# Kernel tuning notes

Measured on AMD Instinct MI355X. Metric: run time of the kernel, lower is better.

Reference implementation:

```python
import jax, jax.numpy as jnp
import numpy as np

D_MODEL = 1024
N_HEADS = 16
D_H = D_MODEL // N_HEADS
MAX_LEN = 2048
BATCH = 2
SEQ = 2048
EPS = 1e-8
W_SCALE = 0.02


def _rms_norm(x, w):
    # RMSNorm: x * rsqrt(mean(x^2) + eps) * w
    ms = jnp.mean(jnp.square(x), axis=-1, keepdims=True)
    return w * (x * jax.lax.rsqrt(ms + EPS))


def setup_inputs() -> dict:
    key = jax.random.key(0)
    ks = jax.random.split(key, 12)
    d = D_MODEL
    inp = {
        "x": jax.random.normal(ks[0], (BATCH, SEQ, d), dtype=jnp.float32),
        "t_bias": jnp.zeros((1,), dtype=jnp.float32),  # unused by the module
        "p_bias": jax.random.normal(ks[1], (MAX_LEN, N_HEADS), dtype=jnp.float32),
        # AMS layer params (Linear stored as [in, out])
        "wq": jax.random.normal(ks[2], (d, d), dtype=jnp.float32) * W_SCALE,
        "bq": jnp.zeros((d,), dtype=jnp.float32),
        "wk": jax.random.normal(ks[3], (d, d), dtype=jnp.float32) * W_SCALE,
        "bk": jnp.zeros((d,), dtype=jnp.float32),
        "wv": jax.random.normal(ks[4], (d, d), dtype=jnp.float32) * W_SCALE,
        "bv": jnp.zeros((d,), dtype=jnp.float32),
        "wu": jax.random.normal(ks[5], (d, d), dtype=jnp.float32) * W_SCALE,
        "bu": jnp.zeros((d,), dtype=jnp.float32),
        "g_ams": jnp.ones((d,), dtype=jnp.float32),   # shared RMSNorm weight in AMSLayer
        # MFFN layer params
        "w0": jax.random.normal(ks[6], (d, d), dtype=jnp.float32) * W_SCALE,
        "b0": jnp.zeros((d,), dtype=jnp.float32),
        "w1": jax.random.normal(ks[7], (d, 2 * d), dtype=jnp.float32) * W_SCALE,
        "b1": jnp.zeros((2 * d,), dtype=jnp.float32),
        "w2": jax.random.normal(ks[8], (d, d), dtype=jnp.float32) * W_SCALE,
        "b2": jnp.zeros((d,), dtype=jnp.float32),
        "g_mffn": jnp.ones((d,), dtype=jnp.float32),
    }
    return inp


def reference(x, t_bias, p_bias, wq, bq, wk, bk, wv, bv, wu, bu, g_ams,
              w0, b0, w1, b1, w2, b2, g_mffn):
    B, S, d = x.shape
    H, dh = N_HEADS, D_H

    # ---- AMS layer ----
    x_norm = _rms_norm(x, g_ams)

    def proj(w, b):
        # [B,S,d] -> [B,H,S,dh]
        return (x_norm @ w + b).reshape(B, S, H, dh).transpose(0, 2, 1, 3)

    q = proj(wq, bq)
    k = proj(wk, bk)
    v = proj(wv, bv)

    scale = 1.0 / np.sqrt(dh).astype(np.float32)
    score = jnp.einsum('bhsd,bhtd->bhst', q, k) * scale
    # additive positional bias: p_bias[:S].T -> [H,S], broadcast over query dim
    score = score + p_bias[:S, :].T[None, :, None, :]

    attn = jax.nn.silu(score)                        # SiLU instead of softmax
    out = jnp.einsum('bhst,bhtd->bhsd', attn, v)
    out = out.transpose(0, 2, 1, 3).reshape(B, S, d)

    u = jax.nn.silu(x_norm @ wu + bu)
    ams_out = _rms_norm(out, g_ams) * u

    # ---- MFFN layer ----
    o = (ams_out @ w0 + b0) + x
    o_norm = _rms_norm(o, g_mffn)
    x12 = o_norm @ w1 + b1
    x1, x2 = jnp.split(x12, 2, axis=-1)
    swiglu = jax.nn.silu(x1) * x2
    return (swiglu @ w2 + b2) + o
```

## Files before the change

### kernel.cpp

```cpp
#include <hip/hip_runtime.h>
#include <stdint.h>
#include <math.h>


#define D    1024
#define NH   16
#define DH   64
#define B_   2
#define S_   2048
#define ROWS 4096
#define LQ   4096
#define EPSR 1e-8f

typedef unsigned short u16;
typedef __attribute__((ext_vector_type(8))) short short8;
typedef __attribute__((ext_vector_type(4))) float f32x4;
typedef __attribute__((ext_vector_type(16))) float f32x16;
typedef __attribute__((ext_vector_type(4))) int int4v;

__device__ __forceinline__ float bf2f(u16 u) {
    union { uint32_t i; float f; } c; c.i = ((uint32_t)u) << 16; return c.f;
}
__device__ __forceinline__ u16 f2bf(float f) {
    union { float f; uint32_t i; } c; c.f = f;
    uint32_t x = c.i;
    x += 0x7fffu + ((x >> 16) & 1u);
    return (u16)(x >> 16);
}
#define LOG2E 1.44269504f
__device__ __forceinline__ float silu_fast(float v) {
    return v * __builtin_amdgcn_rcpf(1.0f + __builtin_amdgcn_exp2f(v * -LOG2E));
}

__global__ __launch_bounds__(256) void transpose_all_kernel(
    const float* __restrict__ wq, const float* __restrict__ wk,
    const float* __restrict__ wv, const float* __restrict__ wu,
    const float* __restrict__ w0, const float* __restrict__ w2,
    const float* __restrict__ w1,
    u16* __restrict__ wT4, u16* __restrict__ w0T,
    u16* __restrict__ w2T, u16* __restrict__ w1T)
{
    const unsigned MI = 1u << 20;
    const int z = blockIdx.z;
    const float* W; u16* WT; int N; int noff = 0;
    switch (z) {
        case 0: W = wq; WT = wT4;          N = 1024; break;
        case 1: W = wk; WT = wT4 + 1 * MI; N = 1024; break;
        case 2: W = wv; WT = wT4 + 2 * MI; N = 1024; break;
        case 3: W = wu; WT = wT4 + 3 * MI; N = 1024; break;
        case 4: W = w0; WT = w0T;          N = 1024; break;
        case 5: W = w2; WT = w2T;          N = 1024; break;
        case 6: W = w1; WT = w1T;          N = 2048; noff = 0;    break;
        default:W = w1; WT = w1T;          N = 2048; noff = 1024; break;
    }
    __shared__ float T[64][65];
    const int tid = threadIdx.x;
    const int n0 = (blockIdx.x << 6) + noff;
    const int k0 = blockIdx.y << 6;
    const int rr = tid >> 4;
    const int cc = (tid & 15) << 2;
#pragma unroll
    for (int l = 0; l < 4; ++l) {
        const int r = rr + (l << 4);
        float4 v = *(const float4*)&W[(size_t)(k0 + r) * N + n0 + cc];
        T[cc + 0][r] = v.x; T[cc + 1][r] = v.y;
        T[cc + 2][r] = v.z; T[cc + 3][r] = v.w;
    }
    __syncthreads();
    const int n  = tid >> 2;
    const int ks = (tid & 3) << 4;
#pragma unroll
    for (int m = 0; m < 4; ++m) {
        const int k = ks + (m << 2);
        float4 v = *(const float4*)&T[n][k];
        ushort4 o;
        o.x = f2bf(v.x); o.y = f2bf(v.y); o.z = f2bf(v.z); o.w = f2bf(v.w);
        *(ushort4*)&WT[(size_t)(n0 + n) * 1024 + k0 + k] = o;
    }
}

__global__ __launch_bounds__(256) void pbt_kernel(
    const float* __restrict__ pb, float* __restrict__ pbT)
{
    const int tid = threadIdx.x;
    const int r = (blockIdx.x << 7) + (tid >> 1);
    const int c0 = (tid & 1) << 3;
    float4 v0 = *(const float4*)&pb[(size_t)r * NH + c0];
    float4 v1 = *(const float4*)&pb[(size_t)r * NH + c0 + 4];
    pbT[(size_t)(c0 + 0) * S_ + r] = v0.x;
    pbT[(size_t)(c0 + 1) * S_ + r] = v0.y;
    pbT[(size_t)(c0 + 2) * S_ + r] = v0.z;
    pbT[(size_t)(c0 + 3) * S_ + r] = v0.w;
    pbT[(size_t)(c0 + 4) * S_ + r] = v1.x;
    pbT[(size_t)(c0 + 5) * S_ + r] = v1.y;
    pbT[(size_t)(c0 + 6) * S_ + r] = v1.z;
    pbT[(size_t)(c0 + 7) * S_ + r] = v1.w;
}

__global__ __launch_bounds__(256) void rmsnorm_kernel(
    const float* __restrict__ inf, const u16* __restrict__ inb, int ldi,
    const float* __restrict__ g,
    const u16* __restrict__ mul, int ldm,
    u16* __restrict__ out, int ldo)
{
    const int row = blockIdx.x;
    const int tid = threadIdx.x;
    const int c = tid << 2;
    float x0, x1, x2, x3;
    if (inb) {
        ushort4 xi = *(const ushort4*)&inb[(size_t)row * ldi + c];
        x0 = bf2f(xi.x); x1 = bf2f(xi.y); x2 = bf2f(xi.z); x3 = bf2f(xi.w);
    } else {
        float4 xi = *(const float4*)&inf[(size_t)row * ldi + c];
        x0 = xi.x; x1 = xi.y; x2 = xi.z; x3 = xi.w;
    }
    float ss = x0*x0 + x1*x1 + x2*x2 + x3*x3;
#pragma unroll
    for (int off = 32; off > 0; off >>= 1) ss += __shfl_down(ss, off, 64);
    __shared__ float red[4];
    if ((tid & 63) == 0) red[tid >> 6] = ss;
    __syncthreads();
    float r = rsqrtf((red[0] + red[1] + red[2] + red[3]) * (1.0f / D) + EPSR);
    float4 gv = *(const float4*)&g[c];
    float v0 = x0 * r * gv.x, v1 = x1 * r * gv.y, v2 = x2 * r * gv.z, v3 = x3 * r * gv.w;
    if (mul) {
        ushort4 mi = *(const ushort4*)&mul[(size_t)row * ldm + c];
        v0 *= bf2f(mi.x); v1 *= bf2f(mi.y); v2 *= bf2f(mi.z); v3 *= bf2f(mi.w);
    }
    ushort4 o;
    o.x = f2bf(v0); o.y = f2bf(v1); o.z = f2bf(v2); o.w = f2bf(v3);
    *(ushort4*)&out[(size_t)row * ldo + c] = o;
}

__global__ __launch_bounds__(256) void gemm128(
    const u16* __restrict__ A, const u16* __restrict__ WT,
    const float* __restrict__ bs0, const float* __restrict__ bs1,
    const float* __restrict__ bs2, const float* __restrict__ bs3,
    u16* __restrict__ outb, int ldo, int actmask,
    u16* __restrict__ VT, int vtsel)
{
    __shared__ u16 As[128 * 32];
    __shared__ u16 Bs[128 * 32];
    const int tid  = threadIdx.x;
    const int wave = tid >> 6;
    const int lane = tid & 63;
    const int lm   = lane & 15;
    const int quad = lane >> 4;
    const int row0 = blockIdx.y << 7;
    const int col0 = blockIdx.x << 7;
    const int wr = (wave >> 1) << 6;
    const int wc = (wave & 1) << 6;

    const int srow = wave * 32 + (lane >> 2);
    const int skp  = (lane & 3) << 3;
    const u16* Ag = A  + (size_t)(row0 + srow) * 1024 + skp;
    const u16* Bg = WT + (size_t)(col0 + srow) * 1024 + skp;
    u16* Asd0 = &As[(wave * 32) * 32];
    u16* Asd1 = &As[(wave * 32 + 16) * 32];
    u16* Bsd0 = &Bs[(wave * 32) * 32];
    u16* Bsd1 = &Bs[(wave * 32 + 16) * 32];

    f32x4 acc[4][4] = {};

    for (int k0 = 0; k0 < 1024; k0 += 32) {
        __syncthreads();
        __builtin_amdgcn_global_load_lds(
            (const __attribute__((address_space(1))) void*)(Ag + k0),
            (__attribute__((address_space(3))) void*)Asd0, 16, 0, 0);
        __builtin_amdgcn_global_load_lds(
            (const __attribute__((address_space(1))) void*)(Ag + 16 * 1024 + k0),
            (__attribute__((address_space(3))) void*)Asd1, 16, 0, 0);
        __builtin_amdgcn_global_load_lds(
            (const __attribute__((address_space(1))) void*)(Bg + k0),
            (__attribute__((address_space(3))) void*)Bsd0, 16, 0, 0);
        __builtin_amdgcn_global_load_lds(
            (const __attribute__((address_space(1))) void*)(Bg + 16 * 1024 + k0),
            (__attribute__((address_space(3))) void*)Bsd1, 16, 0, 0);
        __syncthreads();
        short8 af[4], bf[4];
#pragma unroll
        for (int i = 0; i < 4; ++i)
            af[i] = *(const short8*)&As[(wr + i * 16 + lm) * 32 + quad * 8];
#pragma unroll
        for (int j = 0; j < 4; ++j)
            bf[j] = *(const short8*)&Bs[(wc + j * 16 + lm) * 32 + quad * 8];
#pragma unroll
        for (int i = 0; i < 4; ++i)
#pragma unroll
            for (int j = 0; j < 4; ++j)
                acc[i][j] = __builtin_amdgcn_mfma_f32_16x16x32_bf16(af[i], bf[j], acc[i][j], 0, 0, 0);
    }
    const int sel = col0 >> 10;
    const float* bias = (sel == 0) ? bs0 : (sel == 1) ? bs1 : (sel == 2) ? bs2 : bs3;
    const int act = (actmask >> sel) & 1;
    if (VT && sel == vtsel) {
        const int b = row0 >> 11;
#pragma unroll
        for (int j = 0; j < 4; ++j) {
            const int c2 = (col0 + wc + j * 16 + lm) & 1023;
            const int h  = c2 >> 6;
            const int dh = c2 & 63;
            const float bj = bias[c2];
            u16* vrow = VT + ((size_t)(b * NH + h) * 64 + dh) * (size_t)S_;
#pragma unroll
            for (int i = 0; i < 4; ++i) {
                const int tb = (row0 & 2047) + wr + i * 16 + quad * 4;
                ushort4 o;
                o.x = f2bf(acc[i][j][0] + bj);
                o.y = f2bf(acc[i][j][1] + bj);
                o.z = f2bf(acc[i][j][2] + bj);
                o.w = f2bf(acc[i][j][3] + bj);
                *(ushort4*)&vrow[tb] = o;
            }
        }
    } else {
#pragma unroll
        for (int j = 0; j < 4; ++j) {
            const int colg = col0 + wc + j * 16 + lm;
            const float bj = bias[colg & 1023];
#pragma unroll
            for (int i = 0; i < 4; ++i) {
#pragma unroll
                for (int r = 0; r < 4; ++r) {
                    const int rowg = row0 + wr + i * 16 + quad * 4 + r;
                    float v = acc[i][j][r] + bj;
                    if (act) v = silu_fast(v);
                    outb[(size_t)rowg * ldo + colg] = f2bf(v);
                }
            }
        }
    }
}

__global__ __launch_bounds__(256) void gemm64(
    const u16* __restrict__ A, int lda, const u16* __restrict__ WT,
    const float* __restrict__ bias,
    const float* __restrict__ res,
    float* __restrict__ outf, int ldo)
{
    __shared__ u16 As[128 * 32];
    __shared__ u16 Bs[64 * 32];
    const int tid  = threadIdx.x;
    const int wave = tid >> 6;
    const int lane = tid & 63;
    const int lm   = lane & 15;
    const int quad = lane >> 4;
    const int row0 = blockIdx.y << 7;
    const int col0 = blockIdx.x << 6;
    const int wr = (wave >> 1) << 6;
    const int wc = (wave & 1) << 5;

    const int srA = wave * 32 + (lane >> 2);
    const int srB = wave * 16 + (lane >> 2);
    const int skp = (lane & 3) << 3;
    const u16* Ag = A  + (size_t)(row0 + srA) * lda + skp;
    const u16* Bg = WT + (size_t)(col0 + srB) * 1024 + skp;
    u16* Asd0 = &As[(wave * 32) * 32];
    u16* Asd1 = &As[(wave * 32 + 16) * 32];
    u16* Bsd  = &Bs[(wave * 16) * 32];

    f32x4 acc[4][2] = {};

    for (int k0 = 0; k0 < 1024; k0 += 32) {
        __syncthreads();
        __builtin_amdgcn_global_load_lds(
            (const __attribute__((address_space(1))) void*)(Ag + k0),
            (__attribute__((address_space(3))) void*)Asd0, 16, 0, 0);
        __builtin_amdgcn_global_load_lds(
            (const __attribute__((address_space(1))) void*)(Ag + (size_t)16 * lda + k0),
            (__attribute__((address_space(3))) void*)Asd1, 16, 0, 0);
        __builtin_amdgcn_global_load_lds(
            (const __attribute__((address_space(1))) void*)(Bg + k0),
            (__attribute__((address_space(3))) void*)Bsd, 16, 0, 0);
        __syncthreads();
        short8 af[4], bf[2];
#pragma unroll
        for (int i = 0; i < 4; ++i)
            af[i] = *(const short8*)&As[(wr + i * 16 + lm) * 32 + quad * 8];
#pragma unroll
        for (int j = 0; j < 2; ++j)
            bf[j] = *(const short8*)&Bs[(wc + j * 16 + lm) * 32 + quad * 8];
#pragma unroll
        for (int i = 0; i < 4; ++i)
#pragma unroll
            for (int j = 0; j < 2; ++j)
                acc[i][j] = __builtin_amdgcn_mfma_f32_16x16x32_bf16(af[i], bf[j], acc[i][j], 0, 0, 0);
    }
#pragma unroll
    for (int j = 0; j < 2; ++j) {
        const int colg = col0 + wc + j * 16 + lm;
        const float bj = bias[colg];
#pragma unroll
        for (int i = 0; i < 4; ++i) {
#pragma unroll
            for (int r = 0; r < 4; ++r) {
                const int rowg = row0 + wr + i * 16 + quad * 4 + r;
                const size_t idx = (size_t)rowg * ldo + colg;
                float v = acc[i][j][r] + bj;
                if (res) v += res[idx];
                outf[idx] = v;
            }
        }
    }
}

__global__ __launch_bounds__(256, 4) void attn_mfma(
    const u16* __restrict__ qkvu, const u16* __restrict__ VT,
    const float* __restrict__ pbT, u16* __restrict__ out)
{
    __shared__ u16 Ks[2][64 * 64];
    __shared__ u16 Vs[2][64 * 64];
    __shared__ float pbl[S_];
    const int tid  = threadIdx.x;
    const int wave = tid >> 6;
    const int lane = tid & 63;
    const int l31  = lane & 31;
    const int hi   = lane >> 5;
    const int l7   = lane & 7;
    const int flat = blockIdx.x + (blockIdx.y << 4) + (blockIdx.z << 8);
    const int work = ((flat & 7) << 6) + (flat >> 3);
    const int s0 = (work & 15) << 7;
    const int h  = (work >> 4) & 15;
    const int b  = work >> 8;
    const size_t base = (size_t)b * S_ * LQ + (size_t)h * DH;
    const u16* q  = qkvu + base;
    const u16* kg = qkvu + base + 1024;
    const u16* vt = VT + (size_t)(b * NH + h) * 64 * S_;
    const float* pbh = pbT + (size_t)h * S_;

    for (int i = tid * 4; i < S_; i += 1024)
        *(float4*)&pbl[i] = *(const float4*)&pbh[i];

    const int qrow = s0 + wave * 32 + l31;
    short8 qf[4];
#pragma unroll
    for (int i = 0; i < 4; ++i)
        qf[i] = *(const short8*)&q[(size_t)qrow * LQ + i * 16 + hi * 8];

    const int lr  = lane >> 3;
    const int gch = l7 ^ lr;
    const u16* kg0 = kg + (size_t)(16 * wave + lr) * LQ + gch * 8;
    const u16* vg0 = vt + (size_t)(16 * wave + lr) * S_ + gch * 8;

#define GLDS(gp, lp) __builtin_amdgcn_global_load_lds( \
        (const __attribute__((address_space(1))) void*)(gp), \
        (__attribute__((address_space(3))) void*)(lp), 16, 0, 0)

    GLDS(kg0,                     &Ks[0][(16 * wave) * 64]);
    GLDS(kg0 + (size_t)8 * LQ,    &Ks[0][(16 * wave + 8) * 64]);
    GLDS(vg0,                     &Vs[0][(16 * wave) * 64]);
    GLDS(vg0 + (size_t)8 * S_,    &Vs[0][(16 * wave + 8) * 64]);

    f32x16 accO[2] = {};
    __syncthreads();

    for (int t0 = 0; t0 < S_; t0 += 64) {
        const int ib = (t0 >> 6) & 1;
        const int nb = ib ^ 1;
        if (t0 + 64 < S_) {
            const size_t tn = (size_t)(t0 + 64);
            GLDS(kg0 + tn * LQ,             &Ks[nb][(16 * wave) * 64]);
            GLDS(kg0 + (tn + 8) * LQ,       &Ks[nb][(16 * wave + 8) * 64]);
            GLDS(vg0 + tn,                  &Vs[nb][(16 * wave) * 64]);
            GLDS(vg0 + tn + (size_t)8 * S_, &Vs[nb][(16 * wave + 8) * 64]);
        }
#pragma unroll
        for (int half = 0; half < 2; ++half) {
            const int ts = half << 5;
            f32x16 st = {};
            __builtin_amdgcn_s_setprio(1);
#pragma unroll
            for (int i = 0; i < 4; ++i) {
                short8 kf = *(const short8*)&Ks[ib][(ts + l31) * 64 + (((2 * i + hi) ^ l7) << 3)];
                st = __builtin_amdgcn_mfma_f32_32x32x16_bf16(kf, qf[i], st, 0, 0, 0);
            }
            __builtin_amdgcn_s_setprio(0);
            int pk[8];
#pragma unroll
            for (int g = 0; g < 4; ++g) {
                float4 pbv = *(const float4*)&pbl[t0 + ts + 8 * g + 4 * hi];
                float p0 = silu_fast(fmaf(st[4 * g + 0], 0.125f, pbv.x));
                float p1 = silu_fast(fmaf(st[4 * g + 1], 0.125f, pbv.y));
                float p2 = silu_fast(fmaf(st[4 * g + 2], 0.125f, pbv.z));
                float p3 = silu_fast(fmaf(st[4 * g + 3], 0.125f, pbv.w));
                asm("v_cvt_pk_bf16_f32 %0, %1, %2" : "=v"(pk[2 * g])     : "v"(p0), "v"(p1));
                asm("v_cvt_pk_bf16_f32 %0, %1, %2" : "=v"(pk[2 * g + 1]) : "v"(p2), "v"(p3));
            }
#pragma unroll
            for (int m = 0; m < 2; ++m) {
                int w0 = pk[4 * m + 0], w2 = pk[4 * m + 2];
                int w1 = pk[4 * m + 1], w3 = pk[4 * m + 3];
                asm("v_permlane32_swap_b32 %0, %1" : "+v"(w0), "+v"(w2));
                asm("v_permlane32_swap_b32 %0, %1" : "+v"(w1), "+v"(w3));
                union { int4v i; short8 s; } pa;
                pa.i.x = w0; pa.i.y = w1; pa.i.z = w2; pa.i.w = w3;
                __builtin_amdgcn_s_setprio(1);
#pragma unroll
                for (int n = 0; n < 2; ++n) {
                    short8 vf = *(const short8*)&Vs[ib][(32 * n + l31) * 64 +
                        ((((ts >> 3) + 2 * m + hi) ^ l7) << 3)];
                    accO[n] = __builtin_amdgcn_mfma_f32_32x32x16_bf16(pa.s, vf, accO[n], 0, 0, 0);
                }
                __builtin_amdgcn_s_setprio(0);
            }
        }
        __syncthreads();
    }
#undef GLDS
    const int qb = s0 + wave * 32 + 4 * hi;
#pragma unroll
    for (int n = 0; n < 2; ++n)
#pragma unroll
        for (int r = 0; r < 16; ++r) {
            const int qq = qb + (r & 3) + 8 * (r >> 2);
            out[base + (size_t)qq * LQ + 32 * n + l31] = f2bf(accO[n][r]);
        }
}

__global__ __launch_bounds__(256) void swiglu_kernel(u16* __restrict__ qkvu)
{
    const size_t e = ((size_t)blockIdx.x * 256 + threadIdx.x) << 2;
    const size_t r = e >> 10;
    const int    c = (int)(e & 1023);
    ushort4 a = *(const ushort4*)&qkvu[r * LQ + c];
    ushort4 b = *(const ushort4*)&qkvu[r * LQ + 1024 + c];
    ushort4 o;
    o.x = f2bf(silu_fast(bf2f(a.x)) * bf2f(b.x));
    o.y = f2bf(silu_fast(bf2f(a.y)) * bf2f(b.y));
    o.z = f2bf(silu_fast(bf2f(a.z)) * bf2f(b.z));
    o.w = f2bf(silu_fast(bf2f(a.w)) * bf2f(b.w));
    *(ushort4*)&qkvu[r * LQ + 2048 + c] = o;
}

extern "C" void kernel_launch(void* const* d_in, const int* in_sizes, int n_in,
                              void* d_out, int out_size, void* d_ws, size_t ws_size,
                              hipStream_t stream)
{
    const float* x      = (const float*)d_in[0];
    const float* pb     = (const float*)d_in[2];
    const float* wq     = (const float*)d_in[3];
    const float* bq     = (const float*)d_in[4];
    const float* wk     = (const float*)d_in[5];
    const float* bk     = (const float*)d_in[6];
    const float* wv     = (const float*)d_in[7];
    const float* bv     = (const float*)d_in[8];
    const float* wu     = (const float*)d_in[9];
    const float* bu     = (const float*)d_in[10];
    const float* g_ams  = (const float*)d_in[11];
    const float* w0     = (const float*)d_in[12];
    const float* b0     = (const float*)d_in[13];
    const float* w1     = (const float*)d_in[14];
    const float* b1     = (const float*)d_in[15];
    const float* w2     = (const float*)d_in[16];
    const float* b2     = (const float*)d_in[17];
    const float* g_mffn = (const float*)d_in[18];
    float* OUT = (float*)d_out;
    u16*   VT  = (u16*)d_out;
    float* pbT = (float*)((u16*)d_out + 4 * (1u << 20));

    const size_t MI = 1024 * 1024;
    u16* WS   = (u16*)d_ws;
    u16* wT4  = WS;
    u16* w0T  = WS + 4 * MI;
    u16* w2T  = WS + 5 * MI;
    u16* w1T  = WS + 6 * MI;
    u16* A0   = WS + 8 * MI;
    u16* QKVU = WS + 12 * MI;

    dim3 blk(256);

    transpose_all_kernel<<<dim3(16, 16, 8), blk, 0, stream>>>(
        wq, wk, wv, wu, w0, w2, w1, wT4, w0T, w2T, w1T);
    pbt_kernel<<<16, blk, 0, stream>>>(pb, pbT);

    rmsnorm_kernel<<<ROWS, blk, 0, stream>>>(x, nullptr, D, g_ams, nullptr, 0, A0, D);
    gemm128<<<dim3(32, 32), blk, 0, stream>>>(A0, wT4, bq, bk, bv, bu,
                                              QKVU, LQ, 0b1000, VT, 2);
    attn_mfma<<<dim3(16, 16, 2), blk, 0, stream>>>(QKVU, VT, pbT, QKVU);
    rmsnorm_kernel<<<ROWS, blk, 0, stream>>>(nullptr, QKVU, LQ, g_ams, QKVU + 3072, LQ, A0, D);
    gemm64<<<dim3(16, 32), blk, 0, stream>>>(A0, D, w0T, b0, x, OUT, D);
    rmsnorm_kernel<<<ROWS, blk, 0, stream>>>(OUT, nullptr, D, g_mffn, nullptr, 0, A0, D);
    gemm128<<<dim3(16, 32), blk, 0, stream>>>(A0, w1T, b1, b1 + 1024, b1, b1,
                                              QKVU, LQ, 0, nullptr, -1);
    swiglu_kernel<<<ROWS * D / 1024, blk, 0, stream>>>(QKVU);
    gemm64<<<dim3(16, 32), blk, 0, stream>>>(QKVU + 2048, LQ, w2T, b2, OUT, OUT, D);
    (void)ws_size; (void)in_sizes; (void)n_in; (void)out_size;
}
```

Measured before the change: 343.8 us.

## Deepen attention K/V prefetch to a four-stage LDS ring with explicit vmcnt waits

The SiLU-attention kernel now keeps four K/V tiles in shared memory instead of two. It issues three tiles ahead and replaces the end-of-iteration __syncthreads with a counted s_waitcnt vmcnt plus a barrier at the top of each iteration. The goal is to hide more global-load latency behind the MFMA work. In exchange, per-block LDS grows from about 40KB to about 72KB. That likely drops the number of resident blocks per CU below the launch-bounds target of four, so the cut in latency-hiding occupancy could cancel the deeper prefetch.

```diff
diff --git a/kernel.cpp b/kernel.cpp
--- a/kernel.cpp
+++ b/kernel.cpp
@@ -308,8 +308,8 @@
     const u16* __restrict__ qkvu, const u16* __restrict__ VT,
     const float* __restrict__ pbT, u16* __restrict__ out)
 {
-    __shared__ u16 Ks[2][64 * 64];
-    __shared__ u16 Vs[2][64 * 64];
+    __shared__ u16 Ks[4][64 * 64];
+    __shared__ u16 Vs[4][64 * 64];
     __shared__ float pbl[S_];
     const int tid  = threadIdx.x;
     const int wave = tid >> 6;
@@ -345,25 +345,30 @@
 #define GLDS(gp, lp) __builtin_amdgcn_global_load_lds( \
         (const __attribute__((address_space(1))) void*)(gp), \
         (__attribute__((address_space(3))) void*)(lp), 16, 0, 0)
-
-    GLDS(kg0,                     &Ks[0][(16 * wave) * 64]);
-    GLDS(kg0 + (size_t)8 * LQ,    &Ks[0][(16 * wave + 8) * 64]);
-    GLDS(vg0,                     &Vs[0][(16 * wave) * 64]);
-    GLDS(vg0 + (size_t)8 * S_,    &Vs[0][(16 * wave + 8) * 64]);
+#define ISSUE(j) do { \
+        const int bu = (j) & 3; \
+        const size_t tn = (size_t)(j) << 6; \
+        GLDS(kg0 + tn * LQ,             &Ks[bu][(16 * wave) * 64]); \
+        GLDS(kg0 + (tn + 8) * LQ,       &Ks[bu][(16 * wave + 8) * 64]); \
+        GLDS(vg0 + tn,                  &Vs[bu][(16 * wave) * 64]); \
+        GLDS(vg0 + tn + (size_t)8 * S_, &Vs[bu][(16 * wave + 8) * 64]); \
+    } while (0)
 
     f32x16 accO[2] = {};
     __syncthreads();
 
-    for (int t0 = 0; t0 < S_; t0 += 64) {
-        const int ib = (t0 >> 6) & 1;
-        const int nb = ib ^ 1;
-        if (t0 + 64 < S_) {
-            const size_t tn = (size_t)(t0 + 64);
-            GLDS(kg0 + tn * LQ,             &Ks[nb][(16 * wave) * 64]);
-            GLDS(kg0 + (tn + 8) * LQ,       &Ks[nb][(16 * wave + 8) * 64]);
-            GLDS(vg0 + tn,                  &Vs[nb][(16 * wave) * 64]);
-            GLDS(vg0 + tn + (size_t)8 * S_, &Vs[nb][(16 * wave + 8) * 64]);
-        }
+    ISSUE(0); ISSUE(1); ISSUE(2);
+
+#pragma unroll 1
+    for (int it = 0; it < 32; ++it) {
+        if (it < 30)       asm volatile("s_waitcnt vmcnt(8)" ::: "memory");
+        else if (it == 30) asm volatile("s_waitcnt vmcnt(4)" ::: "memory");
+        else               asm volatile("s_waitcnt vmcnt(0)" ::: "memory");
+        __builtin_amdgcn_s_barrier();
+        asm volatile("" ::: "memory");
+        if (it + 3 < 32) ISSUE(it + 3);
+        const int ib = it & 3;
+        const int t0 = it << 6;
 #pragma unroll
         for (int half = 0; half < 2; ++half) {
             const int ts = half << 5;
@@ -404,8 +409,8 @@
                 __builtin_amdgcn_s_setprio(0);
             }
         }
-        __syncthreads();
-    }
+    }
+#undef ISSUE
 #undef GLDS
     const int qb = s0 + wave * 32 + 4 * hi;
 #pragma unroll
```

After: 343.9 us. Within noise of the previous version (+0.0%).

## Split attention key range across two wave groups and reduce partial outputs in LDS

Applied to the files above, without the earlier changes.

The attention kernel now launches 512 threads per block, organised as two groups of four waves. Each group processes half of the key/value sequence with its own double-buffered LDS tiles. At the end, group 1 writes its partial output accumulators to LDS scratch, and group 0 adds them and stores the result. This halves the serial loop length per wave and adds parallelism, since the grid has only 512 blocks. The costs are doubled LDS for K/V, a final reduction and barrier, and lower occupancy per CU through launch bounds (512,2).

```diff
diff --git a/kernel.cpp b/kernel.cpp
--- a/kernel.cpp
+++ b/kernel.cpp
@@ -304,15 +304,17 @@
     }
 }
 
-__global__ __launch_bounds__(256, 4) void attn_mfma(
+__global__ __launch_bounds__(512, 2) void attn_mfma(
     const u16* __restrict__ qkvu, const u16* __restrict__ VT,
     const float* __restrict__ pbT, u16* __restrict__ out)
 {
-    __shared__ u16 Ks[2][64 * 64];
-    __shared__ u16 Vs[2][64 * 64];
+    __shared__ u16 Ks[2][2][64 * 64];
+    __shared__ u16 Vs[2][2][64 * 64];
     __shared__ float pbl[S_];
     const int tid  = threadIdx.x;
     const int wave = tid >> 6;
+    const int grp  = wave >> 2;
+    const int wq4  = wave & 3;
     const int lane = tid & 63;
     const int l31  = lane & 31;
     const int hi   = lane >> 5;
@@ -328,10 +330,10 @@
     const u16* vt = VT + (size_t)(b * NH + h) * 64 * S_;
     const float* pbh = pbT + (size_t)h * S_;
 
-    for (int i = tid * 4; i < S_; i += 1024)
+    for (int i = tid * 4; i < S_; i += 2048)
         *(float4*)&pbl[i] = *(const float4*)&pbh[i];
 
-    const int qrow = s0 + wave * 32 + l31;
+    const int qrow = s0 + wq4 * 32 + l31;
     short8 qf[4];
 #pragma unroll
     for (int i = 0; i < 4; ++i)
@@ -339,31 +341,30 @@
 
     const int lr  = lane >> 3;
     const int gch = l7 ^ lr;
-    const u16* kg0 = kg + (size_t)(16 * wave + lr) * LQ + gch * 8;
-    const u16* vg0 = vt + (size_t)(16 * wave + lr) * S_ + gch * 8;
+    const u16* kg0 = kg + (size_t)(16 * wq4 + lr) * LQ + gch * 8;
+    const u16* vg0 = vt + (size_t)(16 * wq4 + lr) * S_ + gch * 8;
 
 #define GLDS(gp, lp) __builtin_amdgcn_global_load_lds( \
         (const __attribute__((address_space(1))) void*)(gp), \
         (__attribute__((address_space(3))) void*)(lp), 16, 0, 0)
-
-    GLDS(kg0,                     &Ks[0][(16 * wave) * 64]);
-    GLDS(kg0 + (size_t)8 * LQ,    &Ks[0][(16 * wave + 8) * 64]);
-    GLDS(vg0,                     &Vs[0][(16 * wave) * 64]);
-    GLDS(vg0 + (size_t)8 * S_,    &Vs[0][(16 * wave + 8) * 64]);
+#define ISSUE(it, bu) do { \
+        const size_t tn = ((size_t)(grp) * 16 + (size_t)(it)) << 6; \
+        GLDS(kg0 + tn * LQ,             &Ks[grp][bu][(16 * wq4) * 64]); \
+        GLDS(kg0 + (tn + 8) * LQ,       &Ks[grp][bu][(16 * wq4 + 8) * 64]); \
+        GLDS(vg0 + tn,                  &Vs[grp][bu][(16 * wq4) * 64]); \
+        GLDS(vg0 + tn + (size_t)8 * S_, &Vs[grp][bu][(16 * wq4 + 8) * 64]); \
+    } while (0)
 
     f32x16 accO[2] = {};
+    ISSUE(0, 0);
     __syncthreads();
 
-    for (int t0 = 0; t0 < S_; t0 += 64) {
-        const int ib = (t0 >> 6) & 1;
+#pragma unroll 1
+    for (int it = 0; it < 16; ++it) {
+        const int ib = it & 1;
         const int nb = ib ^ 1;
-        if (t0 + 64 < S_) {
-            const size_t tn = (size_t)(t0 + 64);
-            GLDS(kg0 + tn * LQ,             &Ks[nb][(16 * wave) * 64]);
-            GLDS(kg0 + (tn + 8) * LQ,       &Ks[nb][(16 * wave + 8) * 64]);
-            GLDS(vg0 + tn,                  &Vs[nb][(16 * wave) * 64]);
-            GLDS(vg0 + tn + (size_t)8 * S_, &Vs[nb][(16 * wave + 8) * 64]);
-        }
+        if (it + 1 < 16) ISSUE(it + 1, nb);
+        const int t0 = grp * 1024 + (it << 6);
 #pragma unroll
         for (int half = 0; half < 2; ++half) {
             const int ts = half << 5;
@@ -371,7 +372,7 @@
             __builtin_amdgcn_s_setprio(1);
 #pragma unroll
             for (int i = 0; i < 4; ++i) {
-                short8 kf = *(const short8*)&Ks[ib][(ts + l31) * 64 + (((2 * i + hi) ^ l7) << 3)];
+                short8 kf = *(const short8*)&Ks[grp][ib][(ts + l31) * 64 + (((2 * i + hi) ^ l7) << 3)];
                 st = __builtin_amdgcn_mfma_f32_32x32x16_bf16(kf, qf[i], st, 0, 0, 0);
             }
             __builtin_amdgcn_s_setprio(0);
@@ -397,7 +398,7 @@
                 __builtin_amdgcn_s_setprio(1);
 #pragma unroll
                 for (int n = 0; n < 2; ++n) {
-                    short8 vf = *(const short8*)&Vs[ib][(32 * n + l31) * 64 +
+                    short8 vf = *(const short8*)&Vs[grp][ib][(32 * n + l31) * 64 +
                         ((((ts >> 3) + 2 * m + hi) ^ l7) << 3)];
                     accO[n] = __builtin_amdgcn_mfma_f32_32x32x16_bf16(pa.s, vf, accO[n], 0, 0, 0);
                 }
@@ -406,15 +407,33 @@
         }
         __syncthreads();
     }
+#undef ISSUE
 #undef GLDS
-    const int qb = s0 + wave * 32 + 4 * hi;
-#pragma unroll
-    for (int n = 0; n < 2; ++n)
-#pragma unroll
-        for (int r = 0; r < 16; ++r) {
-            const int qq = qb + (r & 3) + 8 * (r >> 2);
-            out[base + (size_t)qq * LQ + 32 * n + l31] = f2bf(accO[n][r]);
-        }
+    float* scr = (float*)&Ks[0][0][0];
+    const int sl = wq4 * 64 + lane;
+    if (grp == 1) {
+#pragma unroll
+        for (int n = 0; n < 2; ++n)
+#pragma unroll
+            for (int r = 0; r < 16; ++r)
+                scr[(n * 16 + r) * 256 + sl] = accO[n][r];
+    }
+    __syncthreads();
+    if (grp == 0) {
+#pragma unroll
+        for (int n = 0; n < 2; ++n)
+#pragma unroll
+            for (int r = 0; r < 16; ++r)
+                accO[n][r] += scr[(n * 16 + r) * 256 + sl];
+        const int qb = s0 + wq4 * 32 + 4 * hi;
+#pragma unroll
+        for (int n = 0; n < 2; ++n)
+#pragma unroll
+            for (int r = 0; r < 16; ++r) {
+                const int qq = qb + (r & 3) + 8 * (r >> 2);
+                out[base + (size_t)qq * LQ + 32 * n + l31] = f2bf(accO[n][r]);
+            }
+    }
 }
 
 __global__ __launch_bounds__(256) void swiglu_kernel(u16* __restrict__ qkvu)
@@ -476,7 +495,7 @@
     rmsnorm_kernel<<<ROWS, blk, 0, stream>>>(x, nullptr, D, g_ams, nullptr, 0, A0, D);
     gemm128<<<dim3(32, 32), blk, 0, stream>>>(A0, wT4, bq, bk, bv, bu,
                                               QKVU, LQ, 0b1000, VT, 2);
-    attn_mfma<<<dim3(16, 16, 2), blk, 0, stream>>>(QKVU, VT, pbT, QKVU);
+    attn_mfma<<<dim3(16, 16, 2), dim3(512), 0, stream>>>(QKVU, VT, pbT, QKVU);
     rmsnorm_kernel<<<ROWS, blk, 0, stream>>>(nullptr, QKVU, LQ, g_ams, QKVU + 3072, LQ, A0, D);
     gemm64<<<dim3(16, 32), blk, 0, stream>>>(A0, D, w0T, b0, x, OUT, D);
     rmsnorm_kernel<<<ROWS, blk, 0, stream>>>(OUT, nullptr, D, g_mffn, nullptr, 0, A0, D);
```

Measured after the change: 330.6 us. 1.04x faster.
